# Optimization experiments

Hardware: AMD Instinct MI355X
Metric: run time of the kernel (lower is better)

## Reference

```python
import jax, jax.numpy as jnp
import numpy as np

HIDDEN = 1024
INNER = 1024
LR = 0.01
EPS = 1e-5


def _layernorm(x, gamma, beta):
    mu = jnp.mean(x, axis=-1, keepdims=True)
    var = jnp.var(x, axis=-1, keepdims=True)
    return (x - mu) * jax.lax.rsqrt(var + EPS) * gamma + beta


def setup_inputs() -> dict:
    key = jax.random.key(0)
    ks = jax.random.split(key, 8)
    B, S, H, I = 64, 512, HIDDEN, INNER
    x = jax.random.normal(ks[0], (B, S, H), dtype=jnp.float32)
    W_init = jax.random.normal(ks[1], (H, I), dtype=jnp.float32) * 0.02
    b_init = jnp.zeros((I,), dtype=jnp.float32)
    # Linear weights stored as (in, out) so y = x @ W + b
    lim_t = 1.0 / np.sqrt(H)
    Wt = jax.random.uniform(ks[2], (H, I), jnp.float32, -lim_t, lim_t)
    bt = jnp.zeros((I,), dtype=jnp.float32)
    lim_o = 1.0 / np.sqrt(I)
    Wo = jax.random.uniform(ks[3], (I, H), jnp.float32, -lim_o, lim_o)
    bo = jnp.zeros((H,), dtype=jnp.float32)
    lim_g = 1.0 / np.sqrt(2 * H)
    Wg = jax.random.uniform(ks[4], (2 * H, H), jnp.float32, -lim_g, lim_g)
    bg = jnp.zeros((H,), dtype=jnp.float32)
    gamma = jnp.ones((H,), dtype=jnp.float32)
    beta = jnp.zeros((H,), dtype=jnp.float32)
    return {"x": x, "W_init": W_init, "b_init": b_init, "Wt": Wt, "bt": bt,
            "Wo": Wo, "bo": bo, "Wg": Wg, "bg": bg, "gamma": gamma, "beta": beta}


def reference(x, W_init, b_init, Wt, bt, Wo, bo, Wg, bg, gamma, beta):
    B, S, H = x.shape
    I = W_init.shape[1]
    W0 = jnp.broadcast_to(W_init[None], (B, H, I))  # per-batch fast weights
    b0 = jnp.broadcast_to(b_init[None], (B, I))

    def step(carry, x_t):
        W, b = carry
        inner = jnp.einsum('bh,bhi->bi', x_t, W) + b          # [B, I]
        ttt = jax.nn.silu(inner) @ Wo + bo                    # [B, H]
        g = jax.nn.sigmoid(jnp.concatenate([x_t, ttt], axis=-1) @ Wg + bg)
        out = _layernorm(g * ttt + (1.0 - g) * x_t, gamma, beta)
        # test-time training update (target detached)
        target = jax.lax.stop_gradient(x_t @ Wt + bt)
        err = inner - target                                   # [B, I]
        W = W - (LR / I) * x_t[:, :, None] * err[:, None, :]
        b = b - (LR / I) * err
        return (W, b), out

    xs = jnp.swapaxes(x, 0, 1)  # [S, B, H]
    (_, _), ys = jax.lax.scan(step, (W0, b0), xs)
    return jnp.swapaxes(ys, 0, 1)  # [B, S, H]
```

## Files before the change

### kernel.cpp

```cpp
#include <hip/hip_runtime.h>

#define HD 1024
#define ID 1024
#define BATCH 64
#define SEQ 512
#define BS (BATCH*SEQ)
#define CHUNK 64
#define NCHUNK (SEQ/CHUNK)
#define LR_OVER_I (0.01f/1024.0f)

typedef unsigned int u32;
typedef unsigned short ushort_t;
typedef __attribute__((ext_vector_type(8))) short short8;
typedef __attribute__((ext_vector_type(8))) unsigned short ushort8;
typedef __attribute__((ext_vector_type(4))) unsigned short ushort4v;
typedef __attribute__((ext_vector_type(4))) float floatx4;

__device__ inline ushort_t f2bf(float f) {
    union { float f; u32 u; } v; v.f = f;
    return (ushort_t)((v.u + 0x7FFFu + ((v.u >> 16) & 1u)) >> 16);
}
__device__ inline float bf2f(ushort_t h) {
    union { u32 u; float f; } v; v.u = ((u32)h) << 16; return v.f;
}

__device__ inline void load_lds16(const void* g, void* l) {
    __builtin_amdgcn_global_load_lds(
        (const __attribute__((address_space(1))) u32*)g,
        (__attribute__((address_space(3))) u32*)l, 16, 0, 0);
}

__global__ void prep_b(const float* __restrict__ bi, const float* __restrict__ bt,
                       float* __restrict__ bd)
{
    int i = blockIdx.x * 256 + threadIdx.x;
    if (i < ID) bd[i] = bi[i] - bt[i];
}

__global__ void prep_w(const float* __restrict__ Wi, const float* __restrict__ Wt,
                       ushort_t* __restrict__ WdT, ushort_t* __restrict__ WtT)
{
    __shared__ float ti[32][33], tt[32][33];
    int r0 = blockIdx.y * 32, c0 = blockIdx.x * 32;
    for (int i = threadIdx.y; i < 32; i += 8) {
        ti[i][threadIdx.x] = Wi[(long)(r0 + i) * ID + c0 + threadIdx.x];
        tt[i][threadIdx.x] = Wt[(long)(r0 + i) * ID + c0 + threadIdx.x];
    }
    __syncthreads();
    for (int i = threadIdx.y; i < 32; i += 8) {
        float wi = ti[threadIdx.x][i];
        float wt = tt[threadIdx.x][i];
        WdT[(long)(c0 + i) * HD + r0 + threadIdx.x] = f2bf(wi - wt);
        WtT[(long)(c0 + i) * HD + r0 + threadIdx.x] = f2bf(wt);
    }
}

__global__ void transpose_bf16(const float* __restrict__ in, ushort_t* __restrict__ out,
                               int C, int ldo)
{
    __shared__ float t[32][33];
    int r0 = blockIdx.y * 32, c0 = blockIdx.x * 32;
    for (int i = threadIdx.y; i < 32; i += 8)
        t[i][threadIdx.x] = in[(long)(r0 + i) * C + c0 + threadIdx.x];
    __syncthreads();
    for (int i = threadIdx.y; i < 32; i += 8)
        out[(long)(c0 + i) * ldo + r0 + threadIdx.x] = f2bf(t[threadIdx.x][i]);
}

__global__ void convert_bf16(const float* __restrict__ in, ushort_t* __restrict__ out)
{
    long i = ((long)blockIdx.x * 256 + threadIdx.x) * 8;
    float4 a = *(const float4*)(in + i);
    float4 b = *(const float4*)(in + i + 4);
    ushort8 o;
    o[0] = f2bf(a.x); o[1] = f2bf(a.y); o[2] = f2bf(a.z); o[3] = f2bf(a.w);
    o[4] = f2bf(b.x); o[5] = f2bf(b.y); o[6] = f2bf(b.z); o[7] = f2bf(b.w);
    *(ushort8*)(out + i) = o;
}

__global__ __launch_bounds__(256, 3) void gemm_bf16(
    const ushort_t* __restrict__ A0, long sA0, int lda0,
    const ushort_t* __restrict__ A1, long sA1, int lda1,
    const ushort_t* __restrict__ Bt, long sBb, int ldb,
    void* __restrict__ Cv, long sCb, int ldc,
    int KSEG, const float* __restrict__ bias,
    float alpha, float add0, int flags)
{
    int bx, by;
    {
        int L = blockIdx.y * gridDim.x + blockIdx.x;
        if ((gridDim.y & 7) == 0) {
            int xcd = L & 7, g = L >> 3;
            bx = g % gridDim.x;
            by = (g / gridDim.x) * 8 + xcd;
        } else { bx = blockIdx.x; by = blockIdx.y; }
    }
    const int M0 = by * 128, N0 = bx * 128;
    if ((flags & 2) && N0 > M0) return;

    __shared__ ushort_t As[128 * 32];
    __shared__ ushort_t Bs[128 * 32];
    const int tid = threadIdx.x;
    const int wave = tid >> 6, lane = tid & 63;
    const int lr = lane & 15, lq = lane >> 4;
    const int wm = (wave & 1) * 64, wn = (wave >> 1) * 64;

    ushort_t* la0 = &As[(wave * 16)      * 32];
    ushort_t* la1 = &As[(wave * 16 + 64) * 32];
    ushort_t* lb0 = &Bs[(wave * 16)      * 32];
    ushort_t* lb1 = &Bs[(wave * 16 + 64) * 32];

    const ushort_t* gb0 = Bt + (long)blockIdx.z * sBb
                        + (long)(N0 + wave * 16 + (lane >> 2)) * ldb + (lane & 3) * 8;
    const ushort_t* gb1 = gb0 + 64L * ldb;

    floatx4 acc[4][4] = {};

    for (int seg = 0; seg < 2; ++seg) {
        const ushort_t* Ag = (seg == 0) ? A0 : A1;
        if (!Ag) break;
        const int lda = (seg == 0) ? lda0 : lda1;
        Ag += (long)blockIdx.z * ((seg == 0) ? sA0 : sA1);
        const ushort_t* ga0 = Ag + (long)(M0 + wave * 16 + (lane >> 2)) * lda + (lane & 3) * 8;
        const ushort_t* ga1 = ga0 + 64L * lda;

        for (int k0 = 0; k0 < KSEG; k0 += 32) {
            load_lds16(ga0, la0);
            load_lds16(ga1, la1);
            load_lds16(gb0, lb0);
            load_lds16(gb1, lb1);
            ga0 += 32; ga1 += 32; gb0 += 32; gb1 += 32;
            __syncthreads();
            short8 af[4], bf4[4];
#pragma unroll
            for (int i = 0; i < 4; ++i)
                af[i] = *(const short8*)&As[(wm + i * 16 + lr) * 32 + lq * 8];
#pragma unroll
            for (int j = 0; j < 4; ++j)
                bf4[j] = *(const short8*)&Bs[(wn + j * 16 + lr) * 32 + lq * 8];
#pragma unroll
            for (int i = 0; i < 4; ++i)
#pragma unroll
                for (int j = 0; j < 4; ++j)
                    acc[i][j] = __builtin_amdgcn_mfma_f32_16x16x32_bf16(
                        af[i], bf4[j], acc[i][j], 0, 0, 0);
            __syncthreads();
        }
    }

    float bv[4] = {0.f, 0.f, 0.f, 0.f};
    if (bias) {
#pragma unroll
        for (int j = 0; j < 4; ++j) bv[j] = bias[N0 + wn + j * 16 + lr];
    }
    if (flags & 1) {
        ushort_t* C = (ushort_t*)Cv + (long)blockIdx.z * sCb;
#pragma unroll
        for (int i = 0; i < 4; ++i)
#pragma unroll
            for (int r = 0; r < 4; ++r) {
                int row = M0 + wm + i * 16 + lq * 4 + r;
                ushort_t* cp = C + (long)row * ldc + N0 + wn + lr;
#pragma unroll
                for (int j = 0; j < 4; ++j)
                    cp[j * 16] = f2bf(alpha * acc[i][j][r] + add0 + bv[j]);
            }
    } else {
        if ((flags & 8) && wm) return;
        float* C = (float*)Cv + (long)blockIdx.z * sCb;
#pragma unroll
        for (int i = 0; i < 4; ++i)
#pragma unroll
            for (int r = 0; r < 4; ++r) {
                int row = M0 + wm + i * 16 + lq * 4 + r;
                float* cp = C + (long)row * ldc + N0 + wn + lr;
#pragma unroll
                for (int j = 0; j < 4; ++j) {
                    float val = alpha * acc[i][j][r] + add0 + bv[j];
                    if (flags & 4) val += cp[j * 16];
                    cp[j * 16] = val;
                }
            }
    }
}

__global__ __launch_bounds__(256) void intra_solve(float* __restrict__ err,
                                                   const ushort_t* __restrict__ gram,
                                                   ushort_t* __restrict__ ebt, int c)
{
    const int b = blockIdx.x >> 2;
    const int j = ((blockIdx.x & 3) << 8) + threadIdx.x;
    const int t0 = c << 6;
    float* E = err + (long)b * SEQ * ID + (long)t0 * ID + j;
    const ushort_t* Gp = gram + (long)b * SEQ * SEQ + (long)t0 * SEQ + t0;
    __shared__ float Gs[64][64];
    for (int v = threadIdx.x; v < 512; v += 256) {
        int row = v >> 3, col8 = (v & 7) << 3;
        ushort8 g8 = *(const ushort8*)(Gp + (long)row * SEQ + col8);
#pragma unroll
        for (int k = 0; k < 8; ++k) Gs[row][col8 + k] = bf2f(g8[k]);
    }
    __syncthreads();
    float e[64];
    e[0] = E[0];
#pragma unroll
    for (int t = 1; t < 64; ++t) {
        float v = E[(long)t * ID];
        float p0 = 0.f, p1 = 0.f, p2 = 0.f, p3 = 0.f;
#pragma unroll
        for (int s = 0; s + 3 < t; s += 4) {
            p0 = fmaf(Gs[t][s + 0], e[s + 0], p0);
            p1 = fmaf(Gs[t][s + 1], e[s + 1], p1);
            p2 = fmaf(Gs[t][s + 2], e[s + 2], p2);
            p3 = fmaf(Gs[t][s + 3], e[s + 3], p3);
        }
#pragma unroll
        for (int s = t & ~3; s < t; ++s)
            p0 = fmaf(Gs[t][s], e[s], p0);
        float r = v - ((p0 + p1) + (p2 + p3));
        e[t] = r;
        E[(long)t * ID] = r;
    }
    ushort_t* EB = ebt + (long)b * ID * SEQ + (long)j * SEQ + t0;
#pragma unroll
    for (int g = 0; g < 8; ++g) {
        ushort8 o;
#pragma unroll
        for (int k = 0; k < 8; ++k) o[k] = f2bf(e[g * 8 + k]);
        *(ushort8*)(EB + g * 8) = o;
    }
}

__global__ void silu_kernel(const float* __restrict__ err, const ushort_t* __restrict__ tgtb,
                            ushort_t* __restrict__ hb)
{
    long i = ((long)blockIdx.x * 256 + threadIdx.x) * 8;
    float4 e0 = *(const float4*)(err + i);
    float4 e1 = *(const float4*)(err + i + 4);
    ushort8 t8 = *(const ushort8*)(tgtb + i);
    float in[8] = {e0.x + bf2f(t8[0]), e0.y + bf2f(t8[1]),
                   e0.z + bf2f(t8[2]), e0.w + bf2f(t8[3]),
                   e1.x + bf2f(t8[4]), e1.y + bf2f(t8[5]),
                   e1.z + bf2f(t8[6]), e1.w + bf2f(t8[7])};
    ushort8 o;
#pragma unroll
    for (int k = 0; k < 8; ++k) {
        float v = in[k];
        o[k] = f2bf(v / (1.0f + __expf(-v)));
    }
    *(ushort8*)(hb + i) = o;
}

__global__ __launch_bounds__(256) void gate_ln(
    const ushort_t* __restrict__ zb, const ushort_t* __restrict__ tttb,
    const float* __restrict__ x, const float* __restrict__ gamma,
    const float* __restrict__ bet, float* __restrict__ out)
{
    long base = (long)blockIdx.x * HD + threadIdx.x * 4;
    ushort4v zv4 = *(const ushort4v*)(zb + base);
    ushort4v tv4 = *(const ushort4v*)(tttb + base);
    float4 xv = *(const float4*)(x + base);
    float xr[4] = {xv.x, xv.y, xv.z, xv.w};
    float y[4];
#pragma unroll
    for (int k = 0; k < 4; ++k) {
        float g = 1.0f / (1.0f + __expf(-bf2f(zv4[k])));
        float t = bf2f(tv4[k]);
        y[k] = g * t + (1.0f - g) * xr[k];
    }
    float sum = y[0] + y[1] + y[2] + y[3];
    float sq  = y[0]*y[0] + y[1]*y[1] + y[2]*y[2] + y[3]*y[3];
#pragma unroll
    for (int off = 32; off > 0; off >>= 1) {
        sum += __shfl_down(sum, off);
        sq  += __shfl_down(sq, off);
    }
    __shared__ float s1[4], s2[4];
    int wid = threadIdx.x >> 6;
    if ((threadIdx.x & 63) == 0) { s1[wid] = sum; s2[wid] = sq; }
    __syncthreads();
    float tot = s1[0] + s1[1] + s1[2] + s1[3];
    float tsq = s2[0] + s2[1] + s2[2] + s2[3];
    float mu = tot * (1.0f / HD);
    float var = tsq * (1.0f / HD) - mu * mu;
    float rs = rsqrtf(var + 1e-5f);
    int col = threadIdx.x * 4;
    float4 ov;
    ov.x = (y[0] - mu) * rs * gamma[col + 0] + bet[col + 0];
    ov.y = (y[1] - mu) * rs * gamma[col + 1] + bet[col + 1];
    ov.z = (y[2] - mu) * rs * gamma[col + 2] + bet[col + 2];
    ov.w = (y[3] - mu) * rs * gamma[col + 3] + bet[col + 3];
    *(float4*)(out + base) = ov;
}

extern "C" void kernel_launch(void* const* d_in, const int* in_sizes, int n_in,
                              void* d_out, int out_size, void* d_ws, size_t ws_size,
                              hipStream_t stream)
{
    const float* x    = (const float*)d_in[0];
    const float* Wi   = (const float*)d_in[1];
    const float* bi   = (const float*)d_in[2];
    const float* Wt   = (const float*)d_in[3];
    const float* bt   = (const float*)d_in[4];
    const float* Wo   = (const float*)d_in[5];
    const float* bo   = (const float*)d_in[6];
    const float* Wg   = (const float*)d_in[7];
    const float* bg   = (const float*)d_in[8];
    const float* gam  = (const float*)d_in[9];
    const float* bet  = (const float*)d_in[10];
    float* out = (float*)d_out;

    float* u       = (float*)d_ws;
    ushort_t* tgtb = (ushort_t*)(u + (long)BS * ID);
    float* gram    = (float*)(tgtb + (long)BS * ID);
    ushort_t* xb   = (ushort_t*)(gram + (long)BATCH * SEQ * SEQ);
    ushort_t* tttb = xb + (long)BS * HD;
    ushort_t* WdT  = tttb + (long)BS * HD;
    ushort_t* WtT  = WdT + (long)HD * ID;
    ushort_t* WoT  = WtT + (long)HD * ID;
    ushort_t* WgT  = WoT + (long)HD * ID;
    float* bd      = (float*)(WgT + (long)HD * 2 * HD);
    ushort_t* gramb = (ushort_t*)gram;
    ushort_t* ebt   = (ushort_t*)tttb;
    ushort_t* hb    = (ushort_t*)gram;
    ushort_t* zb    = (ushort_t*)u;

    prep_b<<<4, 256, 0, stream>>>(bi, bt, bd);
    prep_w<<<dim3(32, 32), dim3(32, 8), 0, stream>>>(Wi, Wt, WdT, WtT);
    transpose_bf16<<<dim3(32, 32), dim3(32, 8), 0, stream>>>(Wo, WoT, HD, ID);
    transpose_bf16<<<dim3(32, 32), dim3(32, 8), 0, stream>>>(Wg, WgT, HD, 2 * HD);
    transpose_bf16<<<dim3(32, 32), dim3(32, 8), 0, stream>>>(Wg + (long)HD * HD, WgT + HD, HD, 2 * HD);
    convert_bf16<<<16384, 256, 0, stream>>>(x, xb);

    dim3 gBig(ID / 128, BS / 128, 1);
    gemm_bf16<<<gBig, 256, 0, stream>>>(xb, 0, HD, nullptr, 0, 0, WdT, 0, HD,
                                        u, 0, ID, HD, bd, 1.f, 0.f, 0);
    gemm_bf16<<<gBig, 256, 0, stream>>>(xb, 0, HD, nullptr, 0, 0, WtT, 0, HD,
                                        tgtb, 0, ID, HD, bt, 1.f, 0.f, 1);
    gemm_bf16<<<dim3(SEQ / 128, SEQ / 128, BATCH), 256, 0, stream>>>(
        xb, (long)SEQ * HD, HD, nullptr, 0, 0, xb, (long)SEQ * HD, HD,
        gramb, (long)SEQ * SEQ, SEQ, HD, nullptr, LR_OVER_I, LR_OVER_I, 2 | 1);

    for (int c = 0; c < NCHUNK; ++c) {
        if (c > 0) {
            gemm_bf16<<<dim3(ID / 128, 1, BATCH), 256, 0, stream>>>(
                gramb + (long)c * CHUNK * SEQ, (long)SEQ * SEQ, SEQ,
                nullptr, 0, 0,
                ebt, (long)ID * SEQ, SEQ,
                u + (long)c * CHUNK * ID, (long)SEQ * ID, ID,
                c * CHUNK, nullptr, -1.f, 0.f, 4 | 8);
        }
        intra_solve<<<BATCH * 4, 256, 0, stream>>>(u, gramb, ebt, c);
    }

    silu_kernel<<<16384, 256, 0, stream>>>(u, tgtb, hb);
    gemm_bf16<<<gBig, 256, 0, stream>>>(hb, 0, ID, nullptr, 0, 0, WoT, 0, ID,
                                        tttb, 0, HD, ID, bo, 1.f, 0.f, 1);
    gemm_bf16<<<gBig, 256, 0, stream>>>(xb, 0, HD, tttb, 0, HD, WgT, 0, 2 * HD,
                                        zb, 0, HD, HD, bg, 1.f, 0.f, 1);
    gate_ln<<<BS, 256, 0, stream>>>(zb, tttb, x, gam, bet, out);
}
```

Baseline: 1.241 ms.

## Fuse inter-chunk GEMM into chunk solver and batch setup/prep launches

Merges the per-chunk inter-chunk correction GEMM into the triangular solve kernel, so each block first subtracts G·E from prior chunks with MFMA and then runs the intra-chunk solve. It also fuses the two input-projection GEMMs into one launch via a z-dimension switch, and folds the bias and transpose prep kernels into fewer launches. The aim is to remove kernel launch overhead and a round trip of the u chunk through memory. The fused solver uses only 256 blocks, so the inter-chunk GEMM runs at lower parallelism than the earlier separate launch, which used 512 blocks.

```diff
diff --git a/kernel.cpp b/kernel.cpp
--- a/kernel.cpp
+++ b/kernel.cpp
@@ -30,16 +30,15 @@
         (__attribute__((address_space(3))) u32*)l, 16, 0, 0);
 }
 
-__global__ void prep_b(const float* __restrict__ bi, const float* __restrict__ bt,
+__global__ void prep_w(const float* __restrict__ Wi, const float* __restrict__ Wt,
+                       ushort_t* __restrict__ WdT, ushort_t* __restrict__ WtT,
+                       const float* __restrict__ bi, const float* __restrict__ bt,
                        float* __restrict__ bd)
 {
-    int i = blockIdx.x * 256 + threadIdx.x;
-    if (i < ID) bd[i] = bi[i] - bt[i];
-}
-
-__global__ void prep_w(const float* __restrict__ Wi, const float* __restrict__ Wt,
-                       ushort_t* __restrict__ WdT, ushort_t* __restrict__ WtT)
-{
+    if (blockIdx.x == 0 && blockIdx.y == 0) {
+        int t = threadIdx.y * 32 + threadIdx.x;
+        for (int i = t; i < ID; i += 256) bd[i] = bi[i] - bt[i];
+    }
     __shared__ float ti[32][33], tt[32][33];
     int r0 = blockIdx.y * 32, c0 = blockIdx.x * 32;
     for (int i = threadIdx.y; i < 32; i += 8) {
@@ -55,13 +54,17 @@
     }
 }
 
-__global__ void transpose_bf16(const float* __restrict__ in, ushort_t* __restrict__ out,
-                               int C, int ldo)
-{
+__global__ void prep_transposes(const float* __restrict__ Wo, const float* __restrict__ Wg,
+                                ushort_t* __restrict__ WoT, ushort_t* __restrict__ WgT)
+{
+    const float* in; ushort_t* out; int ldo;
+    if (blockIdx.z == 0)      { in = Wo;                   out = WoT;      ldo = ID; }
+    else if (blockIdx.z == 1) { in = Wg;                   out = WgT;      ldo = 2 * HD; }
+    else                      { in = Wg + (long)HD * HD;   out = WgT + HD; ldo = 2 * HD; }
     __shared__ float t[32][33];
     int r0 = blockIdx.y * 32, c0 = blockIdx.x * 32;
     for (int i = threadIdx.y; i < 32; i += 8)
-        t[i][threadIdx.x] = in[(long)(r0 + i) * C + c0 + threadIdx.x];
+        t[i][threadIdx.x] = in[(long)(r0 + i) * HD + c0 + threadIdx.x];
     __syncthreads();
     for (int i = threadIdx.y; i < 32; i += 8)
         out[(long)(c0 + i) * ldo + r0 + threadIdx.x] = f2bf(t[threadIdx.x][i]);
@@ -84,8 +87,16 @@
     const ushort_t* __restrict__ Bt, long sBb, int ldb,
     void* __restrict__ Cv, long sCb, int ldc,
     int KSEG, const float* __restrict__ bias,
-    float alpha, float add0, int flags)
-{
+    float alpha, float add0, int flags,
+    const ushort_t* __restrict__ Bt2, void* __restrict__ Cv2,
+    const float* __restrict__ bias2, int flags2)
+{
+    long zb = blockIdx.z;
+    int fl = flags;
+    if (flags & 16) {
+        zb = 0;
+        if (blockIdx.z == 1) { Bt = Bt2; Cv = Cv2; bias = bias2; fl = flags2; }
+    }
     int bx, by;
     {
         int L = blockIdx.y * gridDim.x + blockIdx.x;
@@ -96,7 +107,7 @@
         } else { bx = blockIdx.x; by = blockIdx.y; }
     }
     const int M0 = by * 128, N0 = bx * 128;
-    if ((flags & 2) && N0 > M0) return;
+    if ((fl & 2) && N0 > M0) return;
 
     __shared__ ushort_t As[128 * 32];
     __shared__ ushort_t Bs[128 * 32];
@@ -110,7 +121,7 @@
     ushort_t* lb0 = &Bs[(wave * 16)      * 32];
     ushort_t* lb1 = &Bs[(wave * 16 + 64) * 32];
 
-    const ushort_t* gb0 = Bt + (long)blockIdx.z * sBb
+    const ushort_t* gb0 = Bt + zb * sBb
                         + (long)(N0 + wave * 16 + (lane >> 2)) * ldb + (lane & 3) * 8;
     const ushort_t* gb1 = gb0 + 64L * ldb;
 
@@ -120,7 +131,7 @@
         const ushort_t* Ag = (seg == 0) ? A0 : A1;
         if (!Ag) break;
         const int lda = (seg == 0) ? lda0 : lda1;
-        Ag += (long)blockIdx.z * ((seg == 0) ? sA0 : sA1);
+        Ag += zb * ((seg == 0) ? sA0 : sA1);
         const ushort_t* ga0 = Ag + (long)(M0 + wave * 16 + (lane >> 2)) * lda + (lane & 3) * 8;
         const ushort_t* ga1 = ga0 + 64L * lda;
 
@@ -153,8 +164,8 @@
 #pragma unroll
         for (int j = 0; j < 4; ++j) bv[j] = bias[N0 + wn + j * 16 + lr];
     }
-    if (flags & 1) {
-        ushort_t* C = (ushort_t*)Cv + (long)blockIdx.z * sCb;
+    if (fl & 1) {
+        ushort_t* C = (ushort_t*)Cv + zb * sCb;
 #pragma unroll
         for (int i = 0; i < 4; ++i)
 #pragma unroll
@@ -166,8 +177,8 @@
                     cp[j * 16] = f2bf(alpha * acc[i][j][r] + add0 + bv[j]);
             }
     } else {
-        if ((flags & 8) && wm) return;
-        float* C = (float*)Cv + (long)blockIdx.z * sCb;
+        if ((fl & 8) && wm) return;
+        float* C = (float*)Cv + zb * sCb;
 #pragma unroll
         for (int i = 0; i < 4; ++i)
 #pragma unroll
@@ -177,30 +188,89 @@
 #pragma unroll
                 for (int j = 0; j < 4; ++j) {
                     float val = alpha * acc[i][j][r] + add0 + bv[j];
-                    if (flags & 4) val += cp[j * 16];
+                    if (fl & 4) val += cp[j * 16];
                     cp[j * 16] = val;
                 }
             }
     }
 }
 
-__global__ __launch_bounds__(256) void intra_solve(float* __restrict__ err,
+__global__ __launch_bounds__(256) void solve_chunk(float* __restrict__ u,
                                                    const ushort_t* __restrict__ gram,
                                                    ushort_t* __restrict__ ebt, int c)
 {
-    const int b = blockIdx.x >> 2;
-    const int j = ((blockIdx.x & 3) << 8) + threadIdx.x;
+    const int b = blockIdx.z;
+    const int j0 = blockIdx.x << 8;
     const int t0 = c << 6;
-    float* E = err + (long)b * SEQ * ID + (long)t0 * ID + j;
-    const ushort_t* Gp = gram + (long)b * SEQ * SEQ + (long)t0 * SEQ + t0;
-    __shared__ float Gs[64][64];
-    for (int v = threadIdx.x; v < 512; v += 256) {
+    const int tid = threadIdx.x;
+    const int wave = tid >> 6, lane = tid & 63;
+    const int lr = lane & 15, lq = lane >> 4;
+
+    __shared__ __align__(16) char smem[4096 + 16384];
+    ushort_t* As = (ushort_t*)smem;
+    ushort_t* Bs = (ushort_t*)(smem + 4096);
+    float* Gs = (float*)smem;
+
+    const ushort_t* Gb = gram + (long)b * SEQ * SEQ + (long)t0 * SEQ;
+    float* Ub = u + (long)b * SEQ * ID + (long)t0 * ID;
+    ushort_t* Eb = ebt + (long)b * ID * SEQ;
+
+    if (c > 0) {
+        const int K = c << 6;
+        floatx4 acc[4][4] = {};
+        const ushort_t* ga = Gb + (long)(wave * 16 + (lane >> 2)) * SEQ + (lane & 3) * 8;
+        const ushort_t* gb = Eb + (long)(j0 + wave * 16 + (lane >> 2)) * SEQ + (lane & 3) * 8;
+        ushort_t* la  = &As[(wave * 16) * 32];
+        ushort_t* lb0 = &Bs[(wave * 16)       * 32];
+        ushort_t* lb1 = &Bs[(64  + wave * 16) * 32];
+        ushort_t* lb2 = &Bs[(128 + wave * 16) * 32];
+        ushort_t* lb3 = &Bs[(192 + wave * 16) * 32];
+        for (int k0 = 0; k0 < K; k0 += 32) {
+            load_lds16(ga, la);
+            load_lds16(gb,             lb0);
+            load_lds16(gb + 64L * SEQ, lb1);
+            load_lds16(gb + 128L * SEQ, lb2);
+            load_lds16(gb + 192L * SEQ, lb3);
+            ga += 32; gb += 32;
+            __syncthreads();
+            short8 af[4], bf4[4];
+#pragma unroll
+            for (int i = 0; i < 4; ++i)
+                af[i] = *(const short8*)&As[(i * 16 + lr) * 32 + lq * 8];
+#pragma unroll
+            for (int j = 0; j < 4; ++j)
+                bf4[j] = *(const short8*)&Bs[(wave * 64 + j * 16 + lr) * 32 + lq * 8];
+#pragma unroll
+            for (int i = 0; i < 4; ++i)
+#pragma unroll
+                for (int j = 0; j < 4; ++j)
+                    acc[i][j] = __builtin_amdgcn_mfma_f32_16x16x32_bf16(
+                        af[i], bf4[j], acc[i][j], 0, 0, 0);
+            __syncthreads();
+        }
+#pragma unroll
+        for (int i = 0; i < 4; ++i)
+#pragma unroll
+            for (int r = 0; r < 4; ++r) {
+                int row = i * 16 + lq * 4 + r;
+                float* up = Ub + (long)row * ID + j0 + wave * 64 + lr;
+#pragma unroll
+                for (int j = 0; j < 4; ++j)
+                    up[j * 16] -= acc[i][j][r];
+            }
+        __syncthreads();
+    }
+
+    for (int v = tid; v < 512; v += 256) {
         int row = v >> 3, col8 = (v & 7) << 3;
-        ushort8 g8 = *(const ushort8*)(Gp + (long)row * SEQ + col8);
-#pragma unroll
-        for (int k = 0; k < 8; ++k) Gs[row][col8 + k] = bf2f(g8[k]);
+        ushort8 g8 = *(const ushort8*)(Gb + (long)row * SEQ + t0 + col8);
+#pragma unroll
+        for (int k = 0; k < 8; ++k) Gs[row * 64 + col8 + k] = bf2f(g8[k]);
     }
     __syncthreads();
+
+    const int j = j0 + tid;
+    float* E = Ub + j;
     float e[64];
     e[0] = E[0];
 #pragma unroll
@@ -209,19 +279,19 @@
         float p0 = 0.f, p1 = 0.f, p2 = 0.f, p3 = 0.f;
 #pragma unroll
         for (int s = 0; s + 3 < t; s += 4) {
-            p0 = fmaf(Gs[t][s + 0], e[s + 0], p0);
-            p1 = fmaf(Gs[t][s + 1], e[s + 1], p1);
-            p2 = fmaf(Gs[t][s + 2], e[s + 2], p2);
-            p3 = fmaf(Gs[t][s + 3], e[s + 3], p3);
+            p0 = fmaf(Gs[t * 64 + s + 0], e[s + 0], p0);
+            p1 = fmaf(Gs[t * 64 + s + 1], e[s + 1], p1);
+            p2 = fmaf(Gs[t * 64 + s + 2], e[s + 2], p2);
+            p3 = fmaf(Gs[t * 64 + s + 3], e[s + 3], p3);
         }
 #pragma unroll
         for (int s = t & ~3; s < t; ++s)
-            p0 = fmaf(Gs[t][s], e[s], p0);
+            p0 = fmaf(Gs[t * 64 + s], e[s], p0);
         float r = v - ((p0 + p1) + (p2 + p3));
         e[t] = r;
         E[(long)t * ID] = r;
     }
-    ushort_t* EB = ebt + (long)b * ID * SEQ + (long)j * SEQ + t0;
+    ushort_t* EB = Eb + (long)j * SEQ + t0;
 #pragma unroll
     for (int g = 0; g < 8; ++g) {
         ushort8 o;
@@ -325,38 +395,29 @@
     ushort_t* hb    = (ushort_t*)gram;
     ushort_t* zb    = (ushort_t*)u;
 
-    prep_b<<<4, 256, 0, stream>>>(bi, bt, bd);
-    prep_w<<<dim3(32, 32), dim3(32, 8), 0, stream>>>(Wi, Wt, WdT, WtT);
-    transpose_bf16<<<dim3(32, 32), dim3(32, 8), 0, stream>>>(Wo, WoT, HD, ID);
-    transpose_bf16<<<dim3(32, 32), dim3(32, 8), 0, stream>>>(Wg, WgT, HD, 2 * HD);
-    transpose_bf16<<<dim3(32, 32), dim3(32, 8), 0, stream>>>(Wg + (long)HD * HD, WgT + HD, HD, 2 * HD);
+    prep_w<<<dim3(32, 32), dim3(32, 8), 0, stream>>>(Wi, Wt, WdT, WtT, bi, bt, bd);
+    prep_transposes<<<dim3(32, 32, 3), dim3(32, 8), 0, stream>>>(Wo, Wg, WoT, WgT);
     convert_bf16<<<16384, 256, 0, stream>>>(x, xb);
 
     dim3 gBig(ID / 128, BS / 128, 1);
-    gemm_bf16<<<gBig, 256, 0, stream>>>(xb, 0, HD, nullptr, 0, 0, WdT, 0, HD,
-                                        u, 0, ID, HD, bd, 1.f, 0.f, 0);
-    gemm_bf16<<<gBig, 256, 0, stream>>>(xb, 0, HD, nullptr, 0, 0, WtT, 0, HD,
-                                        tgtb, 0, ID, HD, bt, 1.f, 0.f, 1);
+    gemm_bf16<<<dim3(ID / 128, BS / 128, 2), 256, 0, stream>>>(
+        xb, 0, HD, nullptr, 0, 0, WdT, 0, HD,
+        u, 0, ID, HD, bd, 1.f, 0.f, 16,
+        WtT, tgtb, bt, 1);
     gemm_bf16<<<dim3(SEQ / 128, SEQ / 128, BATCH), 256, 0, stream>>>(
         xb, (long)SEQ * HD, HD, nullptr, 0, 0, xb, (long)SEQ * HD, HD,
-        gramb, (long)SEQ * SEQ, SEQ, HD, nullptr, LR_OVER_I, LR_OVER_I, 2 | 1);
-
-    for (int c = 0; c < NCHUNK; ++c) {
-        if (c > 0) {
-            gemm_bf16<<<dim3(ID / 128, 1, BATCH), 256, 0, stream>>>(
-                gramb + (long)c * CHUNK * SEQ, (long)SEQ * SEQ, SEQ,
-                nullptr, 0, 0,
-                ebt, (long)ID * SEQ, SEQ,
-                u + (long)c * CHUNK * ID, (long)SEQ * ID, ID,
-                c * CHUNK, nullptr, -1.f, 0.f, 4 | 8);
-        }
-        intra_solve<<<BATCH * 4, 256, 0, stream>>>(u, gramb, ebt, c);
-    }
+        gramb, (long)SEQ * SEQ, SEQ, HD, nullptr, LR_OVER_I, LR_OVER_I, 2 | 1,
+        nullptr, nullptr, nullptr, 0);
+
+    for (int c = 0; c < NCHUNK; ++c)
+        solve_chunk<<<dim3(4, 1, BATCH), 256, 0, stream>>>(u, gramb, ebt, c);
 
     silu_kernel<<<16384, 256, 0, stream>>>(u, tgtb, hb);
     gemm_bf16<<<gBig, 256, 0, stream>>>(hb, 0, ID, nullptr, 0, 0, WoT, 0, ID,
-                                        tttb, 0, HD, ID, bo, 1.f, 0.f, 1);
+                                        tttb, 0, HD, ID, bo, 1.f, 0.f, 1,
+                                        nullptr, nullptr, nullptr, 0);
     gemm_bf16<<<gBig, 256, 0, stream>>>(xb, 0, HD, tttb, 0, HD, WgT, 0, 2 * HD,
-                                        zb, 0, HD, HD, bg, 1.f, 0.f, 1);
+                                        zb, 0, HD, HD, bg, 1.f, 0.f, 1,
+                                        nullptr, nullptr, nullptr, 0);
     gate_ln<<<BS, 256, 0, stream>>>(zb, tttb, x, gam, bet, out);
 }
```

After: 1.093 ms. -11.9%, faster.
